# Performance work log

Hardware: AMD Instinct MI355X
Metric: run time of the kernel (lower is better)

Reference implementation:

```python
import jax, jax.numpy as jnp
import numpy as np

D, NQ, BS, NL, NH, NP, DFF = 256, 900, 8, 4, 8, 4, 1024
HD = D // NH
SHAPES = np.array([[100, 100], [50, 50], [25, 25], [13, 13]], dtype=np.int64)  # (H, W) per level
LSTART = np.concatenate([[0], np.cumsum(SHAPES[:, 0] * SHAPES[:, 1])[:-1]]).astype(np.int64)
LMEM = int((SHAPES[:, 0] * SHAPES[:, 1]).sum())


def layer_norm(x, g, b, eps=1e-5):
    mu = x.mean(-1, keepdims=True)
    var = ((x - mu) ** 2).mean(-1, keepdims=True)
    return (x - mu) * jax.lax.rsqrt(var + eps) * g + b


def _forward(tgt, tgt_query_pos, tgt_reference_points, memory,
             in_proj_w, in_proj_b, out_proj_w, out_proj_b,
             samp_off_w, samp_off_b, attn_w_w, attn_w_b,
             value_proj_w, value_proj_b, output_proj_w, output_proj_b,
             lin1_w, lin1_b, lin2_w, lin2_b,
             norm1_g, norm1_b, norm2_g, norm2_b, norm3_g, norm3_b):
    # ---- self-attention (seq-first, torch nn.MultiheadAttention semantics) ----
    q = tgt + tgt_query_pos  # q = k = with_pos_embed(tgt, pos)
    Wq, Wk, Wv = jnp.split(in_proj_w, 3, 0)
    bq, bk, bv = jnp.split(in_proj_b, 3, 0)
    def heads(x):  # (nq, bs, d) -> (bs, nh, nq, hd)
        return x.reshape(NQ, BS, NH, HD).transpose(1, 2, 0, 3)
    qh = heads(q @ Wq.T + bq)
    kh = heads(q @ Wk.T + bk)
    vh = heads(tgt @ Wv.T + bv)
    attn = jax.nn.softmax(jnp.einsum('bhqd,bhkd->bhqk', qh, kh) / np.float32(np.sqrt(HD)), -1)
    sa = jnp.einsum('bhqk,bhkd->bhqd', attn, vh).transpose(2, 0, 1, 3).reshape(NQ, BS, D)
    sa = sa @ out_proj_w.T + out_proj_b
    t = layer_norm(tgt + sa, norm2_g, norm2_b)

    # ---- MSDeformAttn cross-attention (batch-first internally) ----
    qb = (t + tgt_query_pos).transpose(1, 0, 2)          # (bs, nq, d)
    refb = tgt_reference_points.transpose(1, 0, 2, 3)    # (bs, nq, nl, 2) in [0,1]
    memb = memory.transpose(1, 0, 2)                     # (bs, L, d)
    value = (memb @ value_proj_w.T + value_proj_b).reshape(BS, LMEM, NH, HD)
    off = (qb @ samp_off_w.T + samp_off_b).reshape(BS, NQ, NH, NL, NP, 2)
    aw = jax.nn.softmax((qb @ attn_w_w.T + attn_w_b).reshape(BS, NQ, NH, NL * NP), -1)
    aw = aw.reshape(BS, NQ, NH, NL, NP)
    normz = jnp.asarray(SHAPES[:, ::-1].copy(), dtype=jnp.float32)  # (nl, 2) = [W, H]
    loc = refb[:, :, None, :, None, :] + off / normz[None, None, None, :, None, :]

    out = jnp.zeros((BS, NQ, NH, HD), jnp.float32)
    for l in range(NL):  # fixed small number of pyramid levels
        Hl, Wl = int(SHAPES[l, 0]), int(SHAPES[l, 1])
        s = int(LSTART[l])
        v_l = value[:, s:s + Hl * Wl]  # (bs, Hl*Wl, nh, hd)
        # grid_sample(align_corners=False, padding=zeros) pixel coords
        x = (loc[:, :, :, l, :, 0] * Wl - 0.5).transpose(0, 1, 3, 2).reshape(BS, NQ * NP, NH)
        y = (loc[:, :, :, l, :, 1] * Hl - 0.5).transpose(0, 1, 3, 2).reshape(BS, NQ * NP, NH)
        x0 = jnp.floor(x)
        y0 = jnp.floor(y)
        samp = jnp.zeros((BS, NQ * NP, NH, HD), jnp.float32)
        for dx in (0, 1):
            for dy in (0, 1):
                xc = x0 + dx
                yc = y0 + dy
                w = (1.0 - jnp.abs(x - xc)) * (1.0 - jnp.abs(y - yc))
                valid = (xc >= 0) & (xc < Wl) & (yc >= 0) & (yc < Hl)
                idx = (jnp.clip(yc, 0, Hl - 1) * Wl + jnp.clip(xc, 0, Wl - 1)).astype(jnp.int32)
                g = jnp.take_along_axis(v_l, idx[..., None], axis=1)  # (bs, nq*np, nh, hd)
                samp = samp + jnp.where(valid, w, 0.0)[..., None] * g
        samp = samp.reshape(BS, NQ, NP, NH, HD)
        out = out + jnp.einsum('bqhp,bqphd->bqhd', aw[:, :, :, l], samp)
    ca = (out.reshape(BS, NQ, D) @ output_proj_w.T + output_proj_b).transpose(1, 0, 2)
    t = layer_norm(t + ca, norm1_g, norm1_b)

    # ---- FFN ----
    ffn = jax.nn.relu(t @ lin1_w.T + lin1_b) @ lin2_w.T + lin2_b
    return layer_norm(t + ffn, norm3_g, norm3_b)


def setup_inputs() -> dict:
    key = jax.random.key(0)
    ks = jax.random.split(key, 24)
    r = lambda i, shape, s: jax.random.normal(ks[i], shape, jnp.float32) * s
    return {
        'tgt': r(0, (NQ, BS, D), 1.0),
        'tgt_query_pos': r(1, (NQ, BS, D), 1.0),
        'tgt_reference_points': jax.random.uniform(ks[2], (NQ, BS, NL, 2), jnp.float32),
        'memory': r(3, (LMEM, BS, D), 1.0),
        'spatial_shapes': jnp.asarray(SHAPES),
        'level_start_index': jnp.asarray(LSTART),
        'in_proj_w': r(4, (3 * D, D), 0.02), 'in_proj_b': r(5, (3 * D,), 0.02),
        'out_proj_w': r(6, (D, D), 0.02), 'out_proj_b': r(7, (D,), 0.02),
        'samp_off_w': r(8, (NH * NL * NP * 2, D), 0.01), 'samp_off_b': r(9, (NH * NL * NP * 2,), 0.01),
        'attn_w_w': r(10, (NH * NL * NP, D), 0.02), 'attn_w_b': r(11, (NH * NL * NP,), 0.02),
        'value_proj_w': r(12, (D, D), 0.02), 'value_proj_b': r(13, (D,), 0.02),
        'output_proj_w': r(14, (D, D), 0.02), 'output_proj_b': r(15, (D,), 0.02),
        'lin1_w': r(16, (DFF, D), 0.02), 'lin1_b': r(17, (DFF,), 0.02),
        'lin2_w': r(18, (D, DFF), 0.02), 'lin2_b': r(19, (D,), 0.02),
        'norm1_g': jnp.ones((D,), jnp.float32), 'norm1_b': jnp.zeros((D,), jnp.float32),
        'norm2_g': jnp.ones((D,), jnp.float32), 'norm2_b': jnp.zeros((D,), jnp.float32),
        'norm3_g': jnp.ones((D,), jnp.float32), 'norm3_b': jnp.zeros((D,), jnp.float32),
    }


def reference(tgt, tgt_query_pos, tgt_reference_points, memory, spatial_shapes, level_start_index,
              in_proj_w, in_proj_b, out_proj_w, out_proj_b, samp_off_w, samp_off_b,
              attn_w_w, attn_w_b, value_proj_w, value_proj_b, output_proj_w, output_proj_b,
              lin1_w, lin1_b, lin2_w, lin2_b, norm1_g, norm1_b, norm2_g, norm2_b, norm3_g, norm3_b):
    # spatial_shapes / level_start_index are static level constants (module-level SHAPES/LSTART)
    return _forward(tgt, tgt_query_pos, tgt_reference_points, memory,
                    in_proj_w, in_proj_b, out_proj_w, out_proj_b,
                    samp_off_w, samp_off_b, attn_w_w, attn_w_b,
                    value_proj_w, value_proj_b, output_proj_w, output_proj_b,
                    lin1_w, lin1_b, lin2_w, lin2_b,
                    norm1_g, norm1_b, norm2_g, norm2_b, norm3_g, norm3_b)
```

## Files before the change

kernel.cpp:

```cpp
#include <hip/hip_runtime.h>
#include <hip/hip_bf16.h>


namespace {
constexpr int D_ = 256;
constexpr int NQ_ = 900;
constexpr int BS_ = 8;
constexpr int NH_ = 8;
constexpr int HD_ = 32;
constexpr int DFF_ = 1024;
constexpr int MTOK = NQ_ * BS_;
constexpr int LMEM_ = 13294;
constexpr long T = (long)MTOK * D_;
constexpr float QSC = 0.17677669529663687f;
constexpr int QKS = 512;
}

typedef __attribute__((ext_vector_type(8))) short bf8_t;
typedef __attribute__((ext_vector_type(4))) float f4_t;

#define MFMA16(a, b, c) __builtin_amdgcn_mfma_f32_16x16x32_bf16((a), (b), (c), 0, 0, 0)

__device__ __forceinline__ unsigned short bfbits(float x) {
    union { __hip_bfloat16 h; unsigned short u; } cv;
    cv.h = __float2bfloat16(x);
    return cv.u;
}
__device__ __forceinline__ float bf2f(unsigned short u) {
    union { float f; unsigned v; } cv;
    cv.v = ((unsigned)u) << 16;
    return cv.f;
}

__device__ __forceinline__ void gload16(const unsigned short* g, unsigned short* l) {
    __builtin_amdgcn_global_load_lds(
        (const __attribute__((address_space(1))) unsigned int*)(g),
        (__attribute__((address_space(3))) unsigned int*)(l), 16, 0, 0);
}
__device__ __forceinline__ void gload16f(const float* g, float* l) {
    __builtin_amdgcn_global_load_lds(
        (const __attribute__((address_space(1))) unsigned int*)(g),
        (__attribute__((address_space(3))) unsigned int*)(l), 16, 0, 0);
}

__global__ void conv_weights(
    const float* __restrict__ ipw, const float* __restrict__ opw,
    const float* __restrict__ sow, const float* __restrict__ aww,
    const float* __restrict__ vpw, const float* __restrict__ outpw,
    const float* __restrict__ l1w, const float* __restrict__ l2w,
    const float* __restrict__ ipb, const float* __restrict__ sob,
    const float* __restrict__ awb,
    unsigned short* __restrict__ Wbf, float* __restrict__ biasAll)
{
    if (blockIdx.x == 0) {
        for (int j = threadIdx.x; j < 512; j += 256)
            biasAll[j] = (j < 256) ? ipb[j] * QSC : ipb[j];
        for (int j = threadIdx.x; j < 384; j += 256)
            biasAll[512 + j] = (j < 256) ? sob[j] : awb[j - 256];
    }
    const long idx4 = (long)blockIdx.x * 256 + threadIdx.x;
    if (idx4 >= 253952) return;
    const long e = idx4 * 4;
    const float* src; long off; float sc = 1.f;
    if (e < 196608)      { src = ipw;   off = 0;      if (e < 65536) sc = QSC; }
    else if (e < 262144) { src = opw;   off = 196608; }
    else if (e < 327680) { src = sow;   off = 262144; }
    else if (e < 360448) { src = aww;   off = 327680; }
    else if (e < 425984) { src = vpw;   off = 360448; }
    else if (e < 491520) { src = outpw; off = 425984; }
    else if (e < 753664) { src = l1w;   off = 491520; }
    else                 { src = l2w;   off = 753664; }
    const float4 v = *(const float4*)(src + (e - off));
    union { unsigned short u[4]; uint2 w; } pk;
    pk.u[0] = bfbits(v.x * sc); pk.u[1] = bfbits(v.y * sc);
    pk.u[2] = bfbits(v.z * sc); pk.u[3] = bfbits(v.w * sc);
    *(uint2*)(Wbf + e) = pk.w;
}

template<bool RELU, bool OUTBF16>
__global__ __launch_bounds__(256) void gemm_mfma(
    const unsigned short* __restrict__ A, const unsigned short* __restrict__ W,
    const float* __restrict__ bias, void* __restrict__ C, int M, int N, int K)
{
    __shared__ unsigned short As[128 * 32];
    __shared__ unsigned short Ws[128 * 32];
    const int t = threadIdx.x;
    const long m0 = (long)blockIdx.x * 128;
    const int n0 = blockIdx.y * 128;
    const int row0 = t >> 2;
    const int cgp = (t & 3) ^ ((t >> 2) & 3);
    long ar0 = m0 + row0;        if (ar0 > M - 1) ar0 = M - 1;
    long ar1 = m0 + 64 + row0;   if (ar1 > M - 1) ar1 = M - 1;
    const unsigned short* ga0 = A + ar0 * K + cgp * 8;
    const unsigned short* ga1 = A + ar1 * K + cgp * 8;
    const unsigned short* gw0 = W + (long)(n0 + row0) * K + cgp * 8;
    const unsigned short* gw1 = W + (long)(n0 + 64 + row0) * K + cgp * 8;
    const int lane = t & 63, wave = t >> 6;
    const int c = lane & 15, g = lane >> 4;
    const int wr = wave >> 1, wc = wave & 1;
    const int sws = (g * 8) ^ ((c & 3) * 8);
    f4_t acc[4][4];
#pragma unroll
    for (int i = 0; i < 4; ++i)
#pragma unroll
        for (int j = 0; j < 4; ++j)
            acc[i][j] = f4_t{0.f, 0.f, 0.f, 0.f};

    for (int kb = 0; kb < K; kb += 32) {
        gload16(ga0 + kb, As + t * 8);
        gload16(ga1 + kb, As + 2048 + t * 8);
        gload16(gw0 + kb, Ws + t * 8);
        gload16(gw1 + kb, Ws + 2048 + t * 8);
        __syncthreads();
        bf8_t af[4], bfr[4];
#pragma unroll
        for (int i = 0; i < 4; ++i) {
            af[i] = *(const bf8_t*)(As + (wr * 64 + i * 16 + c) * 32 + sws);
            bfr[i] = *(const bf8_t*)(Ws + (wc * 64 + i * 16 + c) * 32 + sws);
        }
#pragma unroll
        for (int i = 0; i < 4; ++i)
#pragma unroll
            for (int j = 0; j < 4; ++j)
                acc[i][j] = MFMA16(af[i], bfr[j], acc[i][j]);
        __syncthreads();
    }

#pragma unroll
    for (int i = 0; i < 4; ++i) {
        const long rbase = m0 + wr * 64 + i * 16 + 4 * g;
#pragma unroll
        for (int j = 0; j < 4; ++j) {
            const int col = n0 + wc * 64 + j * 16 + c;
            const float bv = bias[col];
#pragma unroll
            for (int r = 0; r < 4; ++r) {
                const long rr = rbase + r;
                if (rr < M) {
                    float v = acc[i][j][r] + bv;
                    if (RELU) v = fmaxf(v, 0.f);
                    if (OUTBF16) ((unsigned short*)C)[rr * N + col] = bfbits(v);
                    else         ((float*)C)[rr * N + col] = v;
                }
            }
        }
    }
}

template<bool OUTBF16>
__global__ __launch_bounds__(256) void gemm_f32d(
    const float* __restrict__ A, const unsigned short* __restrict__ W,
    const float* __restrict__ bias, void* __restrict__ C,
    int M, int N, int K, int R1, int S1, int S2)
{
    __shared__ float Asf[64 * 64];
    __shared__ unsigned short Ws[128 * 64];
    const int t = threadIdx.x;
    const long m0 = (long)blockIdx.x * 64;
    const int n0 = blockIdx.y * 128;
    const float* gA[4];
#pragma unroll
    for (int l = 0; l < 4; ++l) {
        int r = (int)m0 + l * 16 + (t >> 4); if (r > M - 1) r = M - 1;
        const int sp = (t & 15) ^ ((t >> 4) & 15);
        gA[l] = A + ((long)(r / R1) * S1 + (long)(r % R1) * S2) * K + sp * 4;
    }
    const unsigned short* gW[4];
#pragma unroll
    for (int l = 0; l < 4; ++l) {
        const int r = l * 32 + (t >> 3);
        const int sp = (t & 7) ^ (r & 7);
        gW[l] = W + (long)(n0 + r) * K + sp * 8;
    }
    const int lane = t & 63, wave = t >> 6;
    const int c = lane & 15, g = lane >> 4;
    const int wr = wave >> 1, wc = wave & 1;
    f4_t acc[2][4];
#pragma unroll
    for (int i = 0; i < 2; ++i)
#pragma unroll
        for (int j = 0; j < 4; ++j)
            acc[i][j] = f4_t{0.f, 0.f, 0.f, 0.f};

    for (int kb = 0; kb < K; kb += 64) {
#pragma unroll
        for (int l = 0; l < 4; ++l) gload16f(gA[l] + kb, Asf + l * 1024 + t * 4);
#pragma unroll
        for (int l = 0; l < 4; ++l) gload16(gW[l] + kb, Ws + l * 2048 + t * 8);
        __syncthreads();
#pragma unroll
        for (int s = 0; s < 2; ++s) {
            bf8_t af[2], bfr[4];
#pragma unroll
            for (int i = 0; i < 2; ++i) {
                const int row = wr * 32 + i * 16 + c;
                const int sl0 = (s * 8 + 2 * g) ^ (row & 15);
                const int sl1 = (s * 8 + 2 * g + 1) ^ (row & 15);
                const f4_t lo = *(const f4_t*)(Asf + row * 64 + sl0 * 4);
                const f4_t hi = *(const f4_t*)(Asf + row * 64 + sl1 * 4);
                union { bf8_t v; unsigned short u[8]; } pk;
                pk.u[0] = bfbits(lo[0]); pk.u[1] = bfbits(lo[1]);
                pk.u[2] = bfbits(lo[2]); pk.u[3] = bfbits(lo[3]);
                pk.u[4] = bfbits(hi[0]); pk.u[5] = bfbits(hi[1]);
                pk.u[6] = bfbits(hi[2]); pk.u[7] = bfbits(hi[3]);
                af[i] = pk.v;
            }
#pragma unroll
            for (int j = 0; j < 4; ++j) {
                const int row = wc * 64 + j * 16 + c;
                const int sl = (s * 4 + g) ^ (row & 7);
                bfr[j] = *(const bf8_t*)(Ws + row * 64 + sl * 8);
            }
#pragma unroll
            for (int i = 0; i < 2; ++i)
#pragma unroll
                for (int j = 0; j < 4; ++j)
                    acc[i][j] = MFMA16(af[i], bfr[j], acc[i][j]);
        }
        __syncthreads();
    }

#pragma unroll
    for (int i = 0; i < 2; ++i) {
        const long rbase = m0 + wr * 32 + i * 16 + 4 * g;
#pragma unroll
        for (int j = 0; j < 4; ++j) {
            const int col = n0 + wc * 64 + j * 16 + c;
            const float bv = bias[col];
#pragma unroll
            for (int r = 0; r < 4; ++r) {
                const long rr = rbase + r;
                if (rr < M) {
                    float v = acc[i][j][r] + bv;
                    if (OUTBF16) ((unsigned short*)C)[rr * N + col] = bfbits(v);
                    else         ((float*)C)[rr * N + col] = v;
                }
            }
        }
    }
}

template<bool OUTBF16>
__global__ __launch_bounds__(256) void gemm_f32a(
    const float* __restrict__ A, const float* __restrict__ A2,
    const unsigned short* __restrict__ W, const float* __restrict__ bias,
    void* __restrict__ C, int M, int N, int K)
{
    __shared__ unsigned short As[128 * 32];
    __shared__ unsigned short Ws[128 * 32];
    const int t = threadIdx.x;
    const long m0 = (long)blockIdx.x * 128;
    const int n0 = blockIdx.y * 128;
    const int row0 = t >> 2, cg = t & 3;
    const int cgp = cg ^ ((t >> 2) & 3);
    long ar0 = m0 + row0;        if (ar0 > M - 1) ar0 = M - 1;
    long ar1 = m0 + 64 + row0;   if (ar1 > M - 1) ar1 = M - 1;
    const float* Ap0 = A + ar0 * K + cg * 8;
    const float* Ap1 = A + ar1 * K + cg * 8;
    const float* Bp0 = A2 + ar0 * K + cg * 8;
    const float* Bp1 = A2 + ar1 * K + cg * 8;
    const unsigned short* gw0 = W + (long)(n0 + row0) * K + cgp * 8;
    const unsigned short* gw1 = W + (long)(n0 + 64 + row0) * K + cgp * 8;
    unsigned short* la0 = As + row0 * 32 + ((cg * 8) ^ ((row0 & 3) * 8));
    unsigned short* la1 = la0 + 2048;
    const int lane = t & 63, wave = t >> 6;
    const int c = lane & 15, g = lane >> 4;
    const int wr = wave >> 1, wc = wave & 1;
    const int sws = (g * 8) ^ ((c & 3) * 8);
    f4_t acc[4][4];
#pragma unroll
    for (int i = 0; i < 4; ++i)
#pragma unroll
        for (int j = 0; j < 4; ++j)
            acc[i][j] = f4_t{0.f, 0.f, 0.f, 0.f};

    for (int kb = 0; kb < K; kb += 32) {
        gload16(gw0 + kb, Ws + t * 8);
        gload16(gw1 + kb, Ws + 2048 + t * 8);
        const float4 a00 = *(const float4*)(Ap0 + kb);
        const float4 a01 = *(const float4*)(Ap0 + kb + 4);
        const float4 a10 = *(const float4*)(Ap1 + kb);
        const float4 a11 = *(const float4*)(Ap1 + kb + 4);
        const float4 b00 = *(const float4*)(Bp0 + kb);
        const float4 b01 = *(const float4*)(Bp0 + kb + 4);
        const float4 b10 = *(const float4*)(Bp1 + kb);
        const float4 b11 = *(const float4*)(Bp1 + kb + 4);
        union { bf8_t v; unsigned short u[8]; } p0, p1;
        p0.u[0] = bfbits(a00.x + b00.x); p0.u[1] = bfbits(a00.y + b00.y);
        p0.u[2] = bfbits(a00.z + b00.z); p0.u[3] = bfbits(a00.w + b00.w);
        p0.u[4] = bfbits(a01.x + b01.x); p0.u[5] = bfbits(a01.y + b01.y);
        p0.u[6] = bfbits(a01.z + b01.z); p0.u[7] = bfbits(a01.w + b01.w);
        p1.u[0] = bfbits(a10.x + b10.x); p1.u[1] = bfbits(a10.y + b10.y);
        p1.u[2] = bfbits(a10.z + b10.z); p1.u[3] = bfbits(a10.w + b10.w);
        p1.u[4] = bfbits(a11.x + b11.x); p1.u[5] = bfbits(a11.y + b11.y);
        p1.u[6] = bfbits(a11.z + b11.z); p1.u[7] = bfbits(a11.w + b11.w);
        *(bf8_t*)la0 = p0.v;
        *(bf8_t*)la1 = p1.v;
        __syncthreads();
        bf8_t af[4], bfr[4];
#pragma unroll
        for (int i = 0; i < 4; ++i) {
            af[i] = *(const bf8_t*)(As + (wr * 64 + i * 16 + c) * 32 + sws);
            bfr[i] = *(const bf8_t*)(Ws + (wc * 64 + i * 16 + c) * 32 + sws);
        }
#pragma unroll
        for (int i = 0; i < 4; ++i)
#pragma unroll
            for (int j = 0; j < 4; ++j)
                acc[i][j] = MFMA16(af[i], bfr[j], acc[i][j]);
        __syncthreads();
    }

#pragma unroll
    for (int i = 0; i < 4; ++i) {
        const long rbase = m0 + wr * 64 + i * 16 + 4 * g;
#pragma unroll
        for (int j = 0; j < 4; ++j) {
            const int col = n0 + wc * 64 + j * 16 + c;
            const float bv = bias[col];
#pragma unroll
            for (int r = 0; r < 4; ++r) {
                const long rr = rbase + r;
                if (rr < M) {
                    float v = acc[i][j][r] + bv;
                    if (OUTBF16) ((unsigned short*)C)[rr * N + col] = bfbits(v);
                    else         ((float*)C)[rr * N + col] = v;
                }
            }
        }
    }
}

__global__ __launch_bounds__(256) void attn_mfma(
    const unsigned short* __restrict__ Qb, const unsigned short* __restrict__ Kb,
    const unsigned short* __restrict__ Vb, unsigned short* __restrict__ sa)
{
    __shared__ float smemf[2112];
    unsigned short* Ks = (unsigned short*)smemf;
    unsigned short* Vt = (unsigned short*)(smemf + 1024);
    const int t = threadIdx.x;
    const int wave = t >> 6, lane = t & 63;
    const int g = lane >> 4, c = lane & 15;
    const int b = blockIdx.x >> 3, h = blockIdx.x & 7;
    const int q0 = blockIdx.y * 64 + wave * 16;
    const int q = q0 + c;
    const bool qv = q < NQ_;
    const bf8_t qf = *(const bf8_t*)(Qb + ((long)(qv ? q : 0) * BS_ + b) * QKS + h * HD_ + 8 * g);

    f4_t acc0 = {0.f, 0.f, 0.f, 0.f}, acc1 = {0.f, 0.f, 0.f, 0.f};
    float m_run = -1e30f, l_run = 0.f;
    const int sk = t >> 2, sd = (t & 3) * 8;

    for (int kc = 0; kc < NQ_; kc += 64) {
        __syncthreads();
        {
            const int key = kc + sk;
            union { bf8_t v; unsigned short u[8]; } kv, vv;
            if (key < NQ_) {
                kv.v = *(const bf8_t*)(Kb + ((long)key * BS_ + b) * QKS + h * HD_ + sd);
                vv.v = *(const bf8_t*)(Vb + ((long)key * BS_ + b) * D_ + h * HD_ + sd);
            } else {
#pragma unroll
                for (int u = 0; u < 8; ++u) { kv.u[u] = 0; vv.u[u] = 0; }
            }
            *(bf8_t*)(Ks + sk * 32 + sd) = kv.v;
#pragma unroll
            for (int u = 0; u < 8; ++u) {
                const int r = sd + u;
                Vt[r * 64 + (sk ^ ((r & 7) << 3))] = vv.u[u];
            }
        }
        __syncthreads();

        f4_t s[4];
#pragma unroll
        for (int tt = 0; tt < 4; ++tt) {
            const bf8_t kf = *(const bf8_t*)(Ks + (tt * 16 + c) * 32 + 8 * g);
            f4_t z = {0.f, 0.f, 0.f, 0.f};
            s[tt] = MFMA16(kf, qf, z);
        }
        float sv[16];
#pragma unroll
        for (int tt = 0; tt < 4; ++tt)
#pragma unroll
            for (int r = 0; r < 4; ++r) {
                float x = s[tt][r];
                if (kc + tt * 16 + 4 * g + r >= NQ_) x = -1e30f;
                sv[tt * 4 + r] = x;
            }
        float mloc = sv[0];
#pragma unroll
        for (int i = 1; i < 16; ++i) mloc = fmaxf(mloc, sv[i]);
        mloc = fmaxf(mloc, __shfl_xor(mloc, 16));
        mloc = fmaxf(mloc, __shfl_xor(mloc, 32));
        const float mnew = fmaxf(m_run, mloc);
        const float resc = __expf(m_run - mnew);
        float p[16], ls = 0.f;
#pragma unroll
        for (int i = 0; i < 16; ++i) { p[i] = __expf(sv[i] - mnew); ls += p[i]; }
        ls += __shfl_xor(ls, 16);
        ls += __shfl_xor(ls, 32);
        l_run = l_run * resc + ls;
        m_run = mnew;
#pragma unroll
        for (int r = 0; r < 4; ++r) { acc0[r] *= resc; acc1[r] *= resc; }

        unsigned pk[4][2];
#pragma unroll
        for (int tt = 0; tt < 4; ++tt) {
            pk[tt][0] = (unsigned)bfbits(p[tt * 4 + 0]) | ((unsigned)bfbits(p[tt * 4 + 1]) << 16);
            pk[tt][1] = (unsigned)bfbits(p[tt * 4 + 2]) | ((unsigned)bfbits(p[tt * 4 + 3]) << 16);
        }
        const int srcA = ((g & 1) << 5) + c;
        const int srcB = srcA + 16;
#pragma unroll
        for (int kh = 0; kh < 2; ++kh) {
            const unsigned a0 = __shfl(pk[kh * 2][0], srcA), b0_ = __shfl(pk[kh * 2 + 1][0], srcA);
            const unsigned a1 = __shfl(pk[kh * 2][1], srcA), b1_ = __shfl(pk[kh * 2 + 1][1], srcA);
            const unsigned a2 = __shfl(pk[kh * 2][0], srcB), b2_ = __shfl(pk[kh * 2 + 1][0], srcB);
            const unsigned a3 = __shfl(pk[kh * 2][1], srcB), b3_ = __shfl(pk[kh * 2 + 1][1], srcB);
            union { bf8_t v; unsigned u[4]; } pf;
            const bool hi = (g & 2);
            pf.u[0] = hi ? b0_ : a0; pf.u[1] = hi ? b1_ : a1;
            pf.u[2] = hi ? b2_ : a2; pf.u[3] = hi ? b3_ : a3;
            const int kcol = (kh * 32 + 8 * g) ^ ((c & 7) << 3);
            const bf8_t vf0 = *(const bf8_t*)(Vt + c * 64 + kcol);
            const bf8_t vf1 = *(const bf8_t*)(Vt + (16 + c) * 64 + kcol);
            acc0 = MFMA16(vf0, pf.v, acc0);
            acc1 = MFMA16(vf1, pf.v, acc1);
        }
    }

    __syncthreads();
    const float invl = 1.f / l_run;
    float* O = smemf + wave * 528;
#pragma unroll
    for (int r = 0; r < 4; ++r) {
        O[c * 33 + 4 * g + r] = acc0[r] * invl;
        O[c * 33 + 16 + 4 * g + r] = acc1[r] * invl;
    }
    __syncthreads();
    {
        const int ql = lane >> 2, part = lane & 3;
        const int qg = q0 + ql;
        if (qg < NQ_) {
            union { bf8_t v; unsigned short u[8]; } pk;
#pragma unroll
            for (int u = 0; u < 8; ++u) pk.u[u] = bfbits(O[ql * 33 + part * 8 + u]);
            *(bf8_t*)(sa + ((long)qg * BS_ + b) * D_ + h * HD_ + part * 8) = pk.v;
        }
    }
}

__global__ __launch_bounds__(256) void msdeform_kernel(
    const float* __restrict__ oa, const float* __restrict__ refp,
    const unsigned short* __restrict__ val, unsigned short* __restrict__ out)
{
    __shared__ float saw[128];
    __shared__ float redm[8], redi[8];
    __shared__ float swt[128][4];
    __shared__ int sidx[128][4];
    const int bq = blockIdx.x;
    const int b = bq / NQ_, q = bq % NQ_;
    const int t = threadIdx.x;
    if (t < 128) saw[t] = oa[(long)bq * 384 + 256 + t];
    __syncthreads();
    if (t < 8) {
        float mx = -1e30f;
        for (int i = 0; i < 16; ++i) mx = fmaxf(mx, saw[t * 16 + i]);
        float s = 0.f;
        for (int i = 0; i < 16; ++i) s += __expf(saw[t * 16 + i] - mx);
        redm[t] = mx; redi[t] = 1.f / s;
    }
    __syncthreads();
    if (t < 128) {
        const int h = t >> 4, lp = t & 15, l = lp >> 2, p = lp & 3;
        const float aw = __expf(saw[t] - redm[h]) * redi[h];
        const int Wi = (l == 0) ? 100 : (l == 1) ? 50 : (l == 2) ? 25 : 13;
        const int Hi = Wi;
        const int sl = (l == 0) ? 0 : (l == 1) ? 10000 : (l == 2) ? 12500 : 13125;
        const float offx = oa[(long)bq * 384 + h * 32 + l * 8 + p * 2 + 0];
        const float offy = oa[(long)bq * 384 + h * 32 + l * 8 + p * 2 + 1];
        const float refx = refp[(((long)q * BS_ + b) * 4 + l) * 2 + 0];
        const float refy = refp[(((long)q * BS_ + b) * 4 + l) * 2 + 1];
        const float fW = (float)Wi, fH = (float)Hi;
        const float x = (refx + offx / fW) * fW - 0.5f;
        const float y = (refy + offy / fH) * fH - 0.5f;
        const float x0f = floorf(x), y0f = floorf(y);
        const float fx = x - x0f, fy = y - y0f;
        const int ix = (int)x0f, iy = (int)y0f;
        const float wts[4] = {(1.f - fx) * (1.f - fy), fx * (1.f - fy),
                              (1.f - fx) * fy,          fx * fy};
        const int xs[4] = {ix, ix + 1, ix, ix + 1};
        const int ys[4] = {iy, iy, iy + 1, iy + 1};
#pragma unroll
        for (int tap = 0; tap < 4; ++tap) {
            const bool valid = (xs[tap] >= 0) & (xs[tap] < Wi) & (ys[tap] >= 0) & (ys[tap] < Hi);
            const int xc = min(max(xs[tap], 0), Wi - 1);
            const int yc = min(max(ys[tap], 0), Hi - 1);
            swt[t][tap] = valid ? aw * wts[tap] : 0.f;
            sidx[t][tap] = b * LMEM_ + sl + yc * Wi + xc;
        }
    }
    __syncthreads();
    const int h = t >> 5, r = t & 31, qd = r & 7, s = r >> 3;
    float a0 = 0.f, a1 = 0.f, a2 = 0.f, a3 = 0.f;
#pragma unroll
    for (int i = 0; i < 16; ++i) {
        const int j = h * 16 + i;
        const float wv = swt[j][s];
        const long base = (long)sidx[j][s] * D_ + h * HD_ + qd * 4;
        const uint2 raw = *(const uint2*)(val + base);
        a0 += wv * bf2f((unsigned short)(raw.x & 0xffff));
        a1 += wv * bf2f((unsigned short)(raw.x >> 16));
        a2 += wv * bf2f((unsigned short)(raw.y & 0xffff));
        a3 += wv * bf2f((unsigned short)(raw.y >> 16));
    }
    a0 += __shfl_xor(a0, 8); a0 += __shfl_xor(a0, 16);
    a1 += __shfl_xor(a1, 8); a1 += __shfl_xor(a1, 16);
    a2 += __shfl_xor(a2, 8); a2 += __shfl_xor(a2, 16);
    a3 += __shfl_xor(a3, 8); a3 += __shfl_xor(a3, 16);
    if (s == 0) {
        union { unsigned short u[4]; uint2 w; } pk;
        pk.u[0] = bfbits(a0); pk.u[1] = bfbits(a1); pk.u[2] = bfbits(a2); pk.u[3] = bfbits(a3);
        *(uint2*)(out + (long)bq * D_ + h * HD_ + qd * 4) = pk.w;
    }
}

__global__ __launch_bounds__(256) void ln_kernel(
    const float* __restrict__ inA, const float* __restrict__ inB,
    const float* __restrict__ g, const float* __restrict__ be,
    float* __restrict__ out, const float* __restrict__ pos,
    unsigned short* __restrict__ bfOut, int swapB, int bfMode)
{
    const int r = blockIdx.x * 4 + (threadIdx.x >> 6);
    const int lane = threadIdx.x & 63;
    long rb = r;
    if (swapB) rb = (long)(r & 7) * NQ_ + (r >> 3);
    const float4 a4 = *(const float4*)(inA + (long)r * D_ + lane * 4);
    const float4 b4 = *(const float4*)(inB + rb * D_ + lane * 4);
    float x[4] = {a4.x + b4.x, a4.y + b4.y, a4.z + b4.z, a4.w + b4.w};
    float s = x[0] + x[1] + x[2] + x[3];
#pragma unroll
    for (int off = 32; off > 0; off >>= 1) s += __shfl_xor(s, off);
    const float mu = s * (1.f / D_);
    float v = 0.f;
#pragma unroll
    for (int cc = 0; cc < 4; ++cc) { const float dd = x[cc] - mu; v += dd * dd; }
#pragma unroll
    for (int off = 32; off > 0; off >>= 1) v += __shfl_xor(v, off);
    const float rs = rsqrtf(v * (1.f / D_) + 1e-5f);
    const float4 g4 = *(const float4*)(g + lane * 4);
    const float4 e4 = *(const float4*)(be + lane * 4);
    const float gg[4] = {g4.x, g4.y, g4.z, g4.w};
    const float ee[4] = {e4.x, e4.y, e4.z, e4.w};
    float y[4];
#pragma unroll
    for (int cc = 0; cc < 4; ++cc) y[cc] = (x[cc] - mu) * rs * gg[cc] + ee[cc];
    *(float4*)(out + (long)r * D_ + lane * 4) = make_float4(y[0], y[1], y[2], y[3]);
    if (bfMode) {
        float z[4] = {y[0], y[1], y[2], y[3]};
        long er = r;
        if (bfMode == 2) {
            const float4 p4 = *(const float4*)(pos + (long)r * D_ + lane * 4);
            z[0] += p4.x; z[1] += p4.y; z[2] += p4.z; z[3] += p4.w;
            er = (long)(r & 7) * NQ_ + (r >> 3);
        }
        union { unsigned short u[4]; uint2 w; } pk;
        pk.u[0] = bfbits(z[0]); pk.u[1] = bfbits(z[1]);
        pk.u[2] = bfbits(z[2]); pk.u[3] = bfbits(z[3]);
        *(uint2*)(bfOut + er * D_ + lane * 4) = pk.w;
    }
}

extern "C" void kernel_launch(void* const* d_in, const int* in_sizes, int n_in,
                              void* d_out, int out_size, void* d_ws, size_t ws_size,
                              hipStream_t stream) {
    const float* tgt   = (const float*)d_in[0];
    const float* pos   = (const float*)d_in[1];
    const float* refp  = (const float*)d_in[2];
    const float* mem   = (const float*)d_in[3];
    const float* ipw   = (const float*)d_in[6];
    const float* ipb   = (const float*)d_in[7];
    const float* opw   = (const float*)d_in[8];
    const float* opb   = (const float*)d_in[9];
    const float* sow   = (const float*)d_in[10];
    const float* sob   = (const float*)d_in[11];
    const float* aww   = (const float*)d_in[12];
    const float* awb   = (const float*)d_in[13];
    const float* vpw   = (const float*)d_in[14];
    const float* vpb   = (const float*)d_in[15];
    const float* outpw = (const float*)d_in[16];
    const float* outpb = (const float*)d_in[17];
    const float* l1w   = (const float*)d_in[18];
    const float* l1b   = (const float*)d_in[19];
    const float* l2w   = (const float*)d_in[20];
    const float* l2b   = (const float*)d_in[21];
    const float* n1g = (const float*)d_in[22]; const float* n1be = (const float*)d_in[23];
    const float* n2g = (const float*)d_in[24]; const float* n2be = (const float*)d_in[25];
    const float* n3g = (const float*)d_in[26]; const float* n3be = (const float*)d_in[27];

    char* wsb = (char*)d_ws;
    auto alloc = [&](size_t bytes) { char* p = wsb; wsb += (bytes + 255) & ~(size_t)255; return p; };
    unsigned short* Wbf       = (unsigned short*)alloc(1015808 * 2);
    float*          biasAll   = (float*)alloc(896 * 4);
    unsigned short* QK_bf     = (unsigned short*)alloc(T * 4);
    unsigned short* Vb_bf     = (unsigned short*)alloc(T * 2);
    unsigned short* sa_bf     = (unsigned short*)alloc(T * 2);
    float*          saproj    = (float*)alloc(T * 4);
    float*          t1        = (float*)alloc(T * 4);
    unsigned short* qplus2_bf = (unsigned short*)alloc(T * 2);
    float*          oa        = (float*)alloc((long)MTOK * 384 * 4);
    unsigned short* sampo_bf  = (unsigned short*)alloc(T * 2);
    float*          ca        = (float*)alloc(T * 4);
    float*          t2        = (float*)alloc(T * 4);
    unsigned short* t2_bf     = (unsigned short*)alloc(T * 2);
    unsigned short* ffnh_bf   = (unsigned short*)alloc((long)MTOK * DFF_ * 2);
    float*          ffno      = (float*)alloc(T * 4);
    unsigned short* val       = (unsigned short*)alloc((long)BS_ * LMEM_ * D_ * 2);
    const unsigned short* wqk   = Wbf + 0;
    const unsigned short* wv    = Wbf + 131072;
    const unsigned short* wo    = Wbf + 196608;
    const unsigned short* wsoaw = Wbf + 262144;
    const unsigned short* wvp   = Wbf + 360448;
    const unsigned short* wop   = Wbf + 425984;
    const unsigned short* wl1   = Wbf + 491520;
    const unsigned short* wl2   = Wbf + 753664;
    const float* bias_qk = biasAll;
    const float* bias_oa = biasAll + 512;

    const dim3 blk(256);
    const dim3 g_m(57, 2);

    conv_weights<<<992, blk, 0, stream>>>(ipw, opw, sow, aww, vpw, outpw, l1w, l2w,
                                          ipb, sob, awb, Wbf, biasAll);
    gemm_f32a<true><<<dim3(57, 4), blk, 0, stream>>>(tgt, pos, wqk, bias_qk, QK_bf,
                                                     MTOK, QKS, D_);
    gemm_f32d<true><<<dim3(113, 2), blk, 0, stream>>>(tgt, wv, ipb + 2 * D_, Vb_bf,
                                                      MTOK, D_, D_, MTOK, 0, 1);
    attn_mfma<<<dim3(64, 15), blk, 0, stream>>>(QK_bf, QK_bf + 256, Vb_bf, sa_bf);
    gemm_mfma<false, false><<<g_m, blk, 0, stream>>>(sa_bf, wo, opb, saproj, MTOK, D_, D_);
    ln_kernel<<<1800, blk, 0, stream>>>(tgt, saproj, n2g, n2be, t1, pos, qplus2_bf, 0, 2);
    gemm_f32d<true><<<dim3(1662, 2), blk, 0, stream>>>(mem, wvp, vpb, val,
                                                       BS_ * LMEM_, D_, D_, LMEM_, 1, BS_);
    gemm_mfma<false, false><<<dim3(57, 3), blk, 0, stream>>>(qplus2_bf, wsoaw, bias_oa, oa, MTOK, 384, D_);
    msdeform_kernel<<<7200, blk, 0, stream>>>(oa, refp, val, sampo_bf);
    gemm_mfma<false, false><<<g_m, blk, 0, stream>>>(sampo_bf, wop, outpb, ca, MTOK, D_, D_);
    ln_kernel<<<1800, blk, 0, stream>>>(t1, ca, n1g, n1be, t2, nullptr, t2_bf, 1, 1);
    gemm_mfma<true, true><<<dim3(57, 8), blk, 0, stream>>>(t2_bf, wl1, l1b, ffnh_bf, MTOK, DFF_, D_);
    gemm_mfma<false, false><<<g_m, blk, 0, stream>>>(ffnh_bf, wl2, l2b, ffno, MTOK, D_, DFF_);
    ln_kernel<<<1800, blk, 0, stream>>>(t2, ffno, n3g, n3be, (float*)d_out, nullptr, nullptr, 0, 0);
}
```

Measured before the change: 251.6 us.

## Replace value-projection GEMM with persistent double-buffered async-load kernel

Adds a persistent GEMM for the memory value projection. A fixed grid of 256x2 blocks walks 64-row tiles in a strided loop, double-buffering fp32 A and bf16 W tiles in shared memory through async global-to-LDS loads and converting A to bf16 at fragment load time. It aims to overlap global loads with MFMA work and cut launch and tail overhead compared with the previous 1662-block non-persistent kernel. It costs more LDS per block, which lowers occupancy, and relies on hand-written waitcnt and barrier sequencing.

```diff
diff --git a/kernel.cpp b/kernel.cpp
--- a/kernel.cpp
+++ b/kernel.cpp
@@ -14,6 +14,8 @@
 constexpr long T = (long)MTOK * D_;
 constexpr float QSC = 0.17677669529663687f;
 constexpr int QKS = 512;
+constexpr int MVAL = BS_ * LMEM_;
+constexpr int NTILES = (MVAL + 63) / 64;
 }
 
 typedef __attribute__((ext_vector_type(8))) short bf8_t;
@@ -237,6 +239,120 @@
                 }
             }
         }
+    }
+}
+
+__global__ __launch_bounds__(256) void gemm_f32p(
+    const float* __restrict__ A, const unsigned short* __restrict__ W,
+    const float* __restrict__ bias, unsigned short* __restrict__ C)
+{
+    __shared__ float AsD[2][64 * 64];
+    __shared__ unsigned short WsD[2][128 * 64];
+    const int t = threadIdx.x;
+    const int bx = blockIdx.x;
+    const int n0 = blockIdx.y * 128;
+    const int G = gridDim.x;
+    const int myTiles = (NTILES - bx + G - 1) / G;
+    const int nSteps = myTiles * 4;
+
+    const unsigned short* gW[4];
+#pragma unroll
+    for (int l = 0; l < 4; ++l) {
+        const int r = l * 32 + (t >> 3);
+        const int sp = (t & 7) ^ (r & 7);
+        gW[l] = W + (long)(n0 + r) * 256 + sp * 8;
+    }
+    const int rowA = t >> 4;
+    const int spA = (t & 15) ^ rowA;
+
+    auto issueStep = [&](int ls, int buf) {
+        const int tile = bx + (ls >> 2) * G;
+        const int kb = (ls & 3) * 64;
+#pragma unroll
+        for (int l = 0; l < 4; ++l) {
+            int r = tile * 64 + l * 16 + rowA;
+            if (r > MVAL - 1) r = MVAL - 1;
+            const long arow = (long)((unsigned)r % (unsigned)LMEM_) * 8 + (unsigned)r / (unsigned)LMEM_;
+            gload16f(A + arow * 256 + kb + spA * 4, AsD[buf] + l * 1024 + t * 4);
+        }
+#pragma unroll
+        for (int l = 0; l < 4; ++l)
+            gload16(gW[l] + kb, WsD[buf] + l * 2048 + t * 8);
+    };
+
+    const int lane = t & 63, wave = t >> 6;
+    const int c = lane & 15, g = lane >> 4;
+    const int wr = wave >> 1, wc = wave & 1;
+    f4_t acc[2][4];
+
+    issueStep(0, 0);
+    issueStep(1, 1);
+
+    for (int ls = 0; ls < nSteps; ++ls) {
+        const int cur = ls & 1;
+        if ((ls & 3) == 0) {
+#pragma unroll
+            for (int i = 0; i < 2; ++i)
+#pragma unroll
+                for (int j = 0; j < 4; ++j)
+                    acc[i][j] = f4_t{0.f, 0.f, 0.f, 0.f};
+        }
+        asm volatile("s_waitcnt vmcnt(8)" ::: "memory");
+        __builtin_amdgcn_s_barrier();
+        __builtin_amdgcn_sched_barrier(0);
+        const float* Asf = AsD[cur];
+        const unsigned short* Ws = WsD[cur];
+#pragma unroll
+        for (int s = 0; s < 2; ++s) {
+            bf8_t af[2], bfr[4];
+#pragma unroll
+            for (int i = 0; i < 2; ++i) {
+                const int row = wr * 32 + i * 16 + c;
+                const int sl0 = (s * 8 + 2 * g) ^ (row & 15);
+                const int sl1 = (s * 8 + 2 * g + 1) ^ (row & 15);
+                const f4_t lo = *(const f4_t*)(Asf + row * 64 + sl0 * 4);
+                const f4_t hi = *(const f4_t*)(Asf + row * 64 + sl1 * 4);
+                union { bf8_t v; unsigned short u[8]; } pk;
+                pk.u[0] = bfbits(lo[0]); pk.u[1] = bfbits(lo[1]);
+                pk.u[2] = bfbits(lo[2]); pk.u[3] = bfbits(lo[3]);
+                pk.u[4] = bfbits(hi[0]); pk.u[5] = bfbits(hi[1]);
+                pk.u[6] = bfbits(hi[2]); pk.u[7] = bfbits(hi[3]);
+                af[i] = pk.v;
+            }
+#pragma unroll
+            for (int j = 0; j < 4; ++j) {
+                const int row = wc * 64 + j * 16 + c;
+                const int sl = (s * 4 + g) ^ (row & 7);
+                bfr[j] = *(const bf8_t*)(Ws + row * 64 + sl * 8);
+            }
+#pragma unroll
+            for (int i = 0; i < 2; ++i)
+#pragma unroll
+                for (int j = 0; j < 4; ++j)
+                    acc[i][j] = MFMA16(af[i], bfr[j], acc[i][j]);
+        }
+        if ((ls & 3) == 3) {
+            const long m0 = (long)(bx + (ls >> 2) * G) * 64;
+#pragma unroll
+            for (int i = 0; i < 2; ++i) {
+                const long rbase = m0 + wr * 32 + i * 16 + 4 * g;
+#pragma unroll
+                for (int j = 0; j < 4; ++j) {
+                    const int col = n0 + wc * 64 + j * 16 + c;
+                    const float bv = bias[col];
+#pragma unroll
+                    for (int r = 0; r < 4; ++r) {
+                        const long rr = rbase + r;
+                        if (rr < MVAL)
+                            C[rr * 256 + col] = bfbits(acc[i][j][r] + bv);
+                    }
+                }
+            }
+        }
+        __builtin_amdgcn_sched_barrier(0);
+        __builtin_amdgcn_s_barrier();
+        __builtin_amdgcn_sched_barrier(0);
+        if (ls + 2 < nSteps) issueStep(ls + 2, cur);
     }
 }
 
@@ -641,8 +757,7 @@
     attn_mfma<<<dim3(64, 15), blk, 0, stream>>>(QK_bf, QK_bf + 256, Vb_bf, sa_bf);
     gemm_mfma<false, false><<<g_m, blk, 0, stream>>>(sa_bf, wo, opb, saproj, MTOK, D_, D_);
     ln_kernel<<<1800, blk, 0, stream>>>(tgt, saproj, n2g, n2be, t1, pos, qplus2_bf, 0, 2);
-    gemm_f32d<true><<<dim3(1662, 2), blk, 0, stream>>>(mem, wvp, vpb, val,
-                                                       BS_ * LMEM_, D_, D_, LMEM_, 1, BS_);
+    gemm_f32p<<<dim3(256, 2), blk, 0, stream>>>(mem, wvp, vpb, val);
     gemm_mfma<false, false><<<dim3(57, 3), blk, 0, stream>>>(qplus2_bf, wsoaw, bias_oa, oa, MTOK, 384, D_);
     msdeform_kernel<<<7200, blk, 0, stream>>>(oa, refp, val, sampo_bf);
     gemm_mfma<false, false><<<g_m, blk, 0, stream>>>(sampo_bf, wop, outpb, ca, MTOK, D_, D_);
```

Result: slower. 264.5 us (+5.1%).
